# Performance work log

Hardware: AMD Instinct MI355X
Metric: run time of the kernel (lower is better)

Reference implementation:

```python
import jax, jax.numpy as jnp
import numpy as np

BITWIDTH = 8
SCALE = 2.0 ** (BITWIDTH - 1)  # bipolar SC quantization levels


def quantize(v):
    """SourceGen/BSGen over 2^bitwidth cycles converges to the bitwidth-quantized
    bipolar value in [-1, 1]; straight-through estimator keeps grads alive."""
    q = jnp.round(jnp.clip(v, -1.0, 1.0) * SCALE) / SCALE
    return v + jax.lax.stop_gradient(q - v)


def sc_clip(v):
    # non-scaled SC accumulation saturates the bipolar range [-1, 1]
    return jnp.clip(v, -1.0, 1.0)


def fsu_relu(v):
    # FSUReLU on bipolar streams: negative rates -> 0, stays in [0, 1]
    return jnp.clip(v, 0.0, 1.0)


def conv2d(x, w):
    # NCHW conv, padding=1, stride=1 (HUBConv2d / FSUConv2d rate-level math)
    return jax.lax.conv_general_dilated(
        x, w, window_strides=(1, 1), padding=[(1, 1), (1, 1)],
        dimension_numbers=("NCHW", "OIHW", "NCHW"))


def setup_inputs() -> dict:
    key = jax.random.key(0)
    ks = jax.random.split(key, 8)
    B, W, H, Wd = 2048, 10, 10, 11
    cnn_chn, fc_sz, hid, n_cls = 16, 256, 64, 7
    fc3_in = H * Wd * cnn_chn * 2  # 3520
    s = 0.1
    return {
        "x": jax.random.normal(ks[0], (B, W, H, Wd), jnp.float32) * 0.5,
        "conv1_w": jax.random.normal(ks[1], (cnn_chn, 1, 3, 3), jnp.float32) * s,
        "conv2_w": jax.random.normal(ks[2], (cnn_chn * 2, cnn_chn, 3, 3), jnp.float32) * s,
        "fc3_w": jax.random.normal(ks[3], (fc_sz, fc3_in), jnp.float32) * s,
        "w_ih": jax.random.normal(ks[4], (2 * hid, fc_sz), jnp.float32) * s,
        "w_hh": jax.random.normal(ks[5], (2 * hid, hid), jnp.float32) * s,
        "fc5_w": jax.random.normal(ks[6], (n_cls, hid), jnp.float32) * s,
    }


def _forward(x, conv1_w, conv2_w, fc3_w, w_ih, w_hh, fc5_w):
    B = x.shape[0]
    hid = w_hh.shape[1]

    def mgu_cell(x_t, hx):
        # FSUMGUCell, hard nonlinearities (rnn_hard=True)
        gi = x_t @ w_ih.T                         # [B, 2H]
        gh = hx @ w_hh.T                          # [B, 2H]
        gi_f, gi_n = jnp.split(gi, 2, axis=-1)
        gh_f, gh_n = jnp.split(gh, 2, axis=-1)
        forgetgate = jnp.clip(0.5 * (gi_f + gh_f) + 0.5, 0.0, 1.0)  # hard sigmoid
        newgate_prod = forgetgate * gh_n
        newgate = jnp.clip(gi_n + newgate_prod, -1.0, 1.0)          # hard tanh
        forgetgate_inv_prod = (1.0 - forgetgate) * newgate
        forgetgate_prod = forgetgate * hx
        return forgetgate_inv_prod + forgetgate_prod

    def step(hx, x_win):
        xi = quantize(x_win)[:, None, :, :]        # [B,1,10,11] bitstream rate
        a1 = fsu_relu(sc_clip(conv2d(xi, conv1_w)))
        a2 = fsu_relu(sc_clip(conv2d(a1, conv2_w)))
        f = a2.reshape(B, -1)                      # [B, 3520]
        a3 = fsu_relu(sc_clip(f @ fc3_w.T))        # [B, 256]
        hq = quantize(hx)
        hx_new = mgu_cell(a3, hq)
        return hx_new, None

    hx0 = jnp.zeros((B, hid), x.dtype)
    xs = jnp.transpose(x, (1, 0, 2, 3))            # [W, B, 10, 11]
    hx, _ = jax.lax.scan(step, hx0, xs)
    return hx @ fc5_w.T                            # [B, 7] fc5 logits


def reference(x, conv1_w, conv2_w, fc3_w, w_ih, w_hh, fc5_w):
    return _forward(x, conv1_w, conv2_w, fc3_w, w_ih, w_hh, fc5_w)
```

## Files before the change

kernel.cpp:

```cpp
#include <hip/hip_runtime.h>
#include <hip/hip_bf16.h>
#include <cstdint>
#include <cstddef>


typedef __bf16 bf16x8v __attribute__((ext_vector_type(8)));
typedef float  f32x4   __attribute__((ext_vector_type(4)));

#define WAVE_FENCE() asm volatile("s_waitcnt lgkmcnt(0)" ::: "memory")

#define A1_PS 24
#define A1_RS (13 * A1_PS)
#define A1_ZS (12 * A1_RS)
#define A1_BS 3776
#define XQ_BS 176

#define FC3_K 3584

__global__ __launch_bounds__(256) void cvt_w3p_k(
    const float* __restrict__ in, __hip_bfloat16* __restrict__ out)
{
    int idx = blockIdx.x * 256 + threadIdx.x;
    int n = idx / FC3_K, kp = idx % FC3_K;
    int mt = kp >> 9, r = kp & 511;
    int fq = r >> 7, col = (r >> 3) & 15, nt = (r >> 2) & 1, j = r & 3;
    int pixel = mt * 16 + fq * 4 + j, oc = nt * 16 + col;
    float v = (pixel < 110) ? in[n * 3520 + oc * 110 + pixel] : 0.f;
    out[idx] = __float2bfloat16(v);
}

__global__ __launch_bounds__(256) void cvt_w2p_k(
    const float* __restrict__ w2g, __hip_bfloat16* __restrict__ out)
{
    int idx = blockIdx.x * 256 + threadIdx.x;
    int oc = idx / 160, k = idx % 160;
    int koff = k >> 4, ic = k & 15;
    float v = (koff < 9) ? w2g[(oc * 16 + ic) * 9 + koff] : 0.f;
    out[idx] = __float2bfloat16(v);
}

__global__ __launch_bounds__(256) void cvt_wihfrag_k(
    const float* __restrict__ wih, __hip_bfloat16* __restrict__ out)
{
    int idx = blockIdx.x * 256 + threadIdx.x;
    int e = idx & 7, lane = (idx >> 3) & 63, hl = (idx >> 9) & 1;
    int kt = (idx >> 10) & 7, nt = (idx >> 13) & 7;
    int gate = nt * 16 + (lane & 15);
    int k = kt * 32 + (lane >> 4) * 8 + e;
    float v = wih[gate * 256 + k];
    __hip_bfloat16 hi = __float2bfloat16(v);
    out[idx] = hl ? __float2bfloat16(v - __bfloat162float(hi)) : hi;
}

__global__ __launch_bounds__(256) void cvt_whhfrag_k(
    const float* __restrict__ whh, __hip_bfloat16* __restrict__ out)
{
    int idx = blockIdx.x * 256 + threadIdx.x;
    int e = idx & 7, lane = (idx >> 3) & 63, hl = (idx >> 9) & 1;
    int kt = (idx >> 10) & 1, nt = (idx >> 11) & 7;
    int gate = nt * 16 + (lane & 15);
    int k = kt * 32 + (lane >> 4) * 8 + e;
    float v = whh[gate * 64 + k];
    __hip_bfloat16 hi = __float2bfloat16(v);
    out[idx] = hl ? __float2bfloat16(v - __bfloat162float(hi)) : hi;
}

__global__ __launch_bounds__(256) void conv_all_k(
    const float* __restrict__ x, const float* __restrict__ w1g,
    const __hip_bfloat16* __restrict__ w2p,
    __hip_bfloat16* __restrict__ a2p)
{
    __shared__ __hip_bfloat16 a1_s[4 * A1_BS];
    __shared__ float xq_s[4 * XQ_BS];

    const int tid  = threadIdx.x;
    const int wv   = tid >> 6, lane = tid & 63;
    const int t    = blockIdx.x >> 9;
    const int b    = (blockIdx.x & 511) * 4 + wv;
    const int ab   = wv * A1_BS;
    const int xb   = wv * XQ_BS;

    const int fr  = lane & 15, fq = lane >> 4;
    const int fqh = fq >> 1,  icb = (fq & 1) * 8;

    bf16x8v bfrag[5][2];
#pragma unroll
    for (int kt = 0; kt < 5; ++kt)
#pragma unroll
        for (int nt = 0; nt < 2; ++nt)
            bfrag[kt][nt] = *(const bf16x8v*)&w2p[(nt * 16 + fr) * 160 + kt * 32 + fq * 8];

    const int ocp = lane >> 3, pg = lane & 7;
    float w1a[9], w1b[9];
#pragma unroll
    for (int k = 0; k < 9; ++k) {
        w1a[k] = w1g[(2 * ocp) * 9 + k];
        w1b[k] = w1g[(2 * ocp + 1) * 9 + k];
    }

    {
        bf16x8v z = {};
#pragma unroll
        for (int i = 0; i < 8; ++i) {
            int c = lane + i * 64;
            if (c < A1_BS / 8) *(bf16x8v*)&a1_s[ab + c * 8] = z;
        }
        float4 zf = {0.f, 0.f, 0.f, 0.f};
        if (lane < XQ_BS / 4) *(float4*)&xq_s[xb + lane * 4] = zf;
    }
    WAVE_FENCE();

#pragma unroll
    for (int pass = 0; pass < 2; ++pass) {
        int p = pass * 64 + lane;
        if (p < 110) {
            float xv = x[(size_t)b * 1100 + t * 110 + p];
            xv = fminf(fmaxf(xv, -1.f), 1.f);
            xv = rintf(xv * 128.f) * 0.0078125f;
            int h = p / 11, w = p - h * 11;
            xq_s[xb + (h + 1) * 14 + (w + 1)] = xv;
        }
    }
    WAVE_FENCE();

#pragma unroll 2
    for (int i = 0; i < 14; ++i) {
        int p = pg * 14 + i;
        if (p < 110) {
            int h = p / 11, w = p - h * 11;
            const float* xw = &xq_s[xb + h * 14 + w];
            float a0 = 0.f, a1v = 0.f;
#pragma unroll
            for (int dr = 0; dr < 3; ++dr)
#pragma unroll
                for (int dc = 0; dc < 3; ++dc) {
                    float sv = xw[dr * 14 + dc];
                    a0  += w1a[dr * 3 + dc] * sv;
                    a1v += w1b[dr * 3 + dc] * sv;
                }
            a0  = fminf(fmaxf(a0, 0.f), 1.f);
            a1v = fminf(fmaxf(a1v, 0.f), 1.f);
            __hip_bfloat162 pr;
            pr.x = __float2bfloat16(a0);
            pr.y = __float2bfloat16(a1v);
            *(__hip_bfloat162*)&a1_s[ab + (h + 1) * A1_RS + (w + 1) * A1_PS + 2 * ocp] = pr;
        }
    }
    WAVE_FENCE();

    const int d0 = fqh * 24 + icb;
    const int d1 = (fqh ? 312 : 48) + icb;
    const int d2 = 336 + fqh * 24 + icb;
    const int d3 = 624 + fqh * 24 + icb;

#pragma unroll
    for (int m = 0; m < 7; ++m) {
        int p = m * 16 + fr; if (p > 109) p = 109;
        int h = p / 11, w = p - h * 11;
        const int bm = ab + h * A1_RS + w * A1_PS;
        f32x4 acc0 = {0.f, 0.f, 0.f, 0.f}, acc1 = {0.f, 0.f, 0.f, 0.f};
        bf16x8v a;
        a = *(const bf16x8v*)&a1_s[bm + d0];
        acc0 = __builtin_amdgcn_mfma_f32_16x16x32_bf16(a, bfrag[0][0], acc0, 0, 0, 0);
        acc1 = __builtin_amdgcn_mfma_f32_16x16x32_bf16(a, bfrag[0][1], acc1, 0, 0, 0);
        a = *(const bf16x8v*)&a1_s[bm + d1];
        acc0 = __builtin_amdgcn_mfma_f32_16x16x32_bf16(a, bfrag[1][0], acc0, 0, 0, 0);
        acc1 = __builtin_amdgcn_mfma_f32_16x16x32_bf16(a, bfrag[1][1], acc1, 0, 0, 0);
        a = *(const bf16x8v*)&a1_s[bm + d2];
        acc0 = __builtin_amdgcn_mfma_f32_16x16x32_bf16(a, bfrag[2][0], acc0, 0, 0, 0);
        acc1 = __builtin_amdgcn_mfma_f32_16x16x32_bf16(a, bfrag[2][1], acc1, 0, 0, 0);
        a = *(const bf16x8v*)&a1_s[bm + d3];
        acc0 = __builtin_amdgcn_mfma_f32_16x16x32_bf16(a, bfrag[3][0], acc0, 0, 0, 0);
        acc1 = __builtin_amdgcn_mfma_f32_16x16x32_bf16(a, bfrag[3][1], acc1, 0, 0, 0);
        a = *(const bf16x8v*)&a1_s[fqh ? (ab + A1_ZS) : (bm + 672 + icb)];
        acc0 = __builtin_amdgcn_mfma_f32_16x16x32_bf16(a, bfrag[4][0], acc0, 0, 0, 0);
        acc1 = __builtin_amdgcn_mfma_f32_16x16x32_bf16(a, bfrag[4][1], acc1, 0, 0, 0);

        bf16x8v ov;
#pragma unroll
        for (int j = 0; j < 4; ++j) {
            bool valid = (m * 16 + fq * 4 + j) < 110;
            float v0 = valid ? fminf(fmaxf(acc0[j], 0.f), 1.f) : 0.f;
            float v1 = valid ? fminf(fmaxf(acc1[j], 0.f), 1.f) : 0.f;
            ov[j]     = (__bf16)v0;
            ov[4 + j] = (__bf16)v1;
        }
        *(bf16x8v*)&a2p[(size_t)(t * 2048 + b) * FC3_K + m * 512 + lane * 8] = ov;
    }
}

__global__ __launch_bounds__(256) void fc3_all_k(
    const __hip_bfloat16* __restrict__ A,
    const __hip_bfloat16* __restrict__ W,
    __hip_bfloat16* __restrict__ a3)
{
    __shared__ __hip_bfloat16 As[128 * 64];
    __shared__ __hip_bfloat16 Bs[64 * 64];

    const int tid  = threadIdx.x;
    const int wv   = tid >> 6;
    const int lane = tid & 63;
    const int m0 = blockIdx.x * 128, n0 = blockIdx.y * 64;
    const int wr = wv >> 1, wc = wv & 1;

    const int srow   = lane >> 3;
    const int schunk = lane & 7;
    const int swzc   = schunk ^ srow;

    const int fr = lane & 15;
    const int fq = lane >> 4;

    f32x4 acc[4][2];
#pragma unroll
    for (int mi = 0; mi < 4; ++mi)
#pragma unroll
        for (int ni = 0; ni < 2; ++ni)
            acc[mi][ni] = (f32x4){0.f, 0.f, 0.f, 0.f};

    for (int kt = 0; kt < 56; ++kt) {
        const int kb = kt * 64;
#pragma unroll
        for (int i = 0; i < 4; ++i) {
            const int tr = wv * 32 + i * 8;
            const __hip_bfloat16* srcA =
                A + (size_t)(m0 + tr + srow) * FC3_K + kb + swzc * 8;
            __builtin_amdgcn_global_load_lds(
                (const __attribute__((address_space(1))) void*)srcA,
                (__attribute__((address_space(3))) void*)&As[tr * 64], 16, 0, 0);
        }
#pragma unroll
        for (int i = 0; i < 2; ++i) {
            const int tr = wv * 16 + i * 8;
            const __hip_bfloat16* srcB =
                W + (size_t)(n0 + tr + srow) * FC3_K + kb + swzc * 8;
            __builtin_amdgcn_global_load_lds(
                (const __attribute__((address_space(1))) void*)srcB,
                (__attribute__((address_space(3))) void*)&Bs[tr * 64], 16, 0, 0);
        }
        __syncthreads();

#pragma unroll
        for (int kk = 0; kk < 2; ++kk) {
            bf16x8v af[4], bfv[2];
#pragma unroll
            for (int mi = 0; mi < 4; ++mi) {
                const int rr = wr * 64 + mi * 16 + fr;
                const int cc = (kk * 4 + fq) ^ (rr & 7);
                af[mi] = *(const bf16x8v*)&As[rr * 64 + cc * 8];
            }
#pragma unroll
            for (int ni = 0; ni < 2; ++ni) {
                const int rr = wc * 32 + ni * 16 + fr;
                const int cc = (kk * 4 + fq) ^ (rr & 7);
                bfv[ni] = *(const bf16x8v*)&Bs[rr * 64 + cc * 8];
            }
#pragma unroll
            for (int mi = 0; mi < 4; ++mi)
#pragma unroll
                for (int ni = 0; ni < 2; ++ni)
                    acc[mi][ni] = __builtin_amdgcn_mfma_f32_16x16x32_bf16(
                        af[mi], bfv[ni], acc[mi][ni], 0, 0, 0);
        }
        __syncthreads();
    }

#pragma unroll
    for (int mi = 0; mi < 4; ++mi)
#pragma unroll
        for (int ni = 0; ni < 2; ++ni)
#pragma unroll
            for (int j = 0; j < 4; ++j) {
                int row = m0 + wr * 64 + mi * 16 + fq * 4 + j;
                int col = n0 + wc * 32 + ni * 16 + fr;
                float v = fminf(fmaxf(acc[mi][ni][j], 0.f), 1.f);
                a3[(size_t)row * 256 + col] = __float2bfloat16(v);
            }
}

__global__ __launch_bounds__(256, 1) void mgu_all_k(
    const __hip_bfloat16* __restrict__ a3,
    const __hip_bfloat16* __restrict__ wfi, const __hip_bfloat16* __restrict__ wfh,
    const float* __restrict__ w5, float* __restrict__ out)
{
    __shared__ __hip_bfloat16 a3_s[16 * 256];
    __shared__ __hip_bfloat16 hq_s[16 * 64];
    __shared__ float hx_s[16 * 64];
    __shared__ float w5_s[7 * 64];

    const int tid = threadIdx.x;
    const int wv  = tid >> 6, lane = tid & 63;
    const int fr  = lane & 15, fq = lane >> 4;
    const int b0  = blockIdx.x * 16;
    const int ntf = wv, ntn = wv + 4;

    bf16x8v wiF[8][2], wiN[8][2], whF[2][2], whN[2][2];
#pragma unroll
    for (int kt = 0; kt < 8; ++kt)
#pragma unroll
        for (int hl = 0; hl < 2; ++hl) {
            wiF[kt][hl] = *(const bf16x8v*)&wfi[(((ntf * 8 + kt) * 2 + hl) * 64 + lane) * 8];
            wiN[kt][hl] = *(const bf16x8v*)&wfi[(((ntn * 8 + kt) * 2 + hl) * 64 + lane) * 8];
        }
#pragma unroll
    for (int kt = 0; kt < 2; ++kt)
#pragma unroll
        for (int hl = 0; hl < 2; ++hl) {
            whF[kt][hl] = *(const bf16x8v*)&wfh[(((ntf * 2 + kt) * 2 + hl) * 64 + lane) * 8];
            whN[kt][hl] = *(const bf16x8v*)&wfh[(((ntn * 2 + kt) * 2 + hl) * 64 + lane) * 8];
        }

    for (int i = tid; i < 16 * 64; i += 256) hx_s[i] = 0.f;
    for (int i = tid; i < 7 * 64; i += 256) w5_s[i] = w5[i];
    __syncthreads();

    for (int t = 0; t < 10; ++t) {
#pragma unroll
        for (int pass = 0; pass < 2; ++pass) {
            int i = pass * 256 + tid;
            int r = i >> 5, cq = i & 31;
            bf16x8v v = *(const bf16x8v*)&a3[((size_t)(t * 2048 + b0 + r)) * 256 + cq * 8];
            *(bf16x8v*)&a3_s[r * 256 + ((cq ^ (r & 7)) * 8)] = v;
        }
#pragma unroll
        for (int pass = 0; pass < 4; ++pass) {
            int i = pass * 256 + tid;
            int r = i >> 6, c = i & 63;
            float v = hx_s[r * 64 + c];
            v = fminf(fmaxf(v, -1.f), 1.f);
            v = rintf(v * 128.f) * 0.0078125f;
            hq_s[r * 64 + (((c >> 3) ^ (r & 7)) << 3) + (c & 7)] = __float2bfloat16(v);
        }
        __syncthreads();

        f32x4 accF  = {0.f, 0.f, 0.f, 0.f};
        f32x4 accNi = {0.f, 0.f, 0.f, 0.f};
        f32x4 accNh = {0.f, 0.f, 0.f, 0.f};
#pragma unroll
        for (int kt = 0; kt < 8; ++kt) {
            bf16x8v a = *(const bf16x8v*)&a3_s[fr * 256 + (((kt * 4 + fq) ^ (fr & 7)) * 8)];
            accF  = __builtin_amdgcn_mfma_f32_16x16x32_bf16(a, wiF[kt][0], accF, 0, 0, 0);
            accF  = __builtin_amdgcn_mfma_f32_16x16x32_bf16(a, wiF[kt][1], accF, 0, 0, 0);
            accNi = __builtin_amdgcn_mfma_f32_16x16x32_bf16(a, wiN[kt][0], accNi, 0, 0, 0);
            accNi = __builtin_amdgcn_mfma_f32_16x16x32_bf16(a, wiN[kt][1], accNi, 0, 0, 0);
        }
#pragma unroll
        for (int kt = 0; kt < 2; ++kt) {
            bf16x8v a = *(const bf16x8v*)&hq_s[fr * 64 + (((kt * 4 + fq) ^ (fr & 7)) * 8)];
            accF  = __builtin_amdgcn_mfma_f32_16x16x32_bf16(a, whF[kt][0], accF, 0, 0, 0);
            accF  = __builtin_amdgcn_mfma_f32_16x16x32_bf16(a, whF[kt][1], accF, 0, 0, 0);
            accNh = __builtin_amdgcn_mfma_f32_16x16x32_bf16(a, whN[kt][0], accNh, 0, 0, 0);
            accNh = __builtin_amdgcn_mfma_f32_16x16x32_bf16(a, whN[kt][1], accNh, 0, 0, 0);
        }

        const int j5 = wv * 16 + fr;
#pragma unroll
        for (int j = 0; j < 4; ++j) {
            int b = fq * 4 + j;
            float f = fminf(fmaxf(0.5f * accF[j] + 0.5f, 0.f), 1.f);
            float n = fminf(fmaxf(accNi[j] + f * accNh[j], -1.f), 1.f);
            float hq = __bfloat162float(
                hq_s[b * 64 + ((((j5) >> 3) ^ (b & 7)) << 3) + (j5 & 7)]);
            hx_s[b * 64 + j5] = (1.f - f) * n + f * hq;
        }
        __syncthreads();
    }

    if (tid < 112) {
        int b = tid / 7, c = tid % 7;
        float acc = 0.f;
#pragma unroll
        for (int k = 0; k < 64; ++k) acc += hx_s[b * 64 + k] * w5_s[c * 64 + k];
        out[(size_t)(b0 + b) * 7 + c] = acc;
    }
}

extern "C" void kernel_launch(void* const* d_in, const int* in_sizes, int n_in,
                              void* d_out, int out_size, void* d_ws, size_t ws_size,
                              hipStream_t stream)
{
    const float* x    = (const float*)d_in[0];
    const float* w1   = (const float*)d_in[1];
    const float* w2   = (const float*)d_in[2];
    const float* fc3w = (const float*)d_in[3];
    const float* wih  = (const float*)d_in[4];
    const float* whh  = (const float*)d_in[5];
    const float* fc5w = (const float*)d_in[6];
    float* out = (float*)d_out;

    char* ws = (char*)d_ws;
    __hip_bfloat16* a2p = (__hip_bfloat16*)ws;
    __hip_bfloat16* a3  = (__hip_bfloat16*)(ws + 146800640);
    __hip_bfloat16* w3p = (__hip_bfloat16*)(ws + 157286400);
    __hip_bfloat16* w2p = (__hip_bfloat16*)(ws + 159121408);
    __hip_bfloat16* wfi = (__hip_bfloat16*)(ws + 159131648);
    __hip_bfloat16* wfh = (__hip_bfloat16*)(ws + 159262720);

    cvt_w3p_k<<<3584, 256, 0, stream>>>(fc3w, w3p);
    cvt_w2p_k<<<20, 256, 0, stream>>>(w2, w2p);
    cvt_wihfrag_k<<<256, 256, 0, stream>>>(wih, wfi);
    cvt_whhfrag_k<<<64, 256, 0, stream>>>(whh, wfh);

    conv_all_k<<<5120, 256, 0, stream>>>(x, w1, w2p, a2p);
    fc3_all_k<<<dim3(160, 4), 256, 0, stream>>>(a2p, w3p, a3);
    mgu_all_k<<<128, 256, 0, stream>>>(a3, wfi, wfh, fc5w, out);
}
```

Baseline: 120.8 us.

## Double-buffer fc3 GEMM loads, fuse weight conversions, row-tile conv1, swap grid order

The fc3 GEMM now double-buffers its LDS tiles, issuing the next k-tile's direct-to-LDS loads before computing the current one and waiting with vmcnt. This overlaps global memory latency with MFMA work. The four weight-conversion kernels are merged into one launch to cut launch overhead. conv1 now computes whole output rows per lane from vectorised float4 row loads instead of scattered per-pixel reads. The fc3 grid is transposed so the four N-blocks sharing an A tile run adjacently, improving L2 reuse; LDS use doubles.

```diff
diff --git a/kernel.cpp b/kernel.cpp
--- a/kernel.cpp
+++ b/kernel.cpp
@@ -13,56 +13,53 @@
 #define A1_RS (13 * A1_PS)
 #define A1_ZS (12 * A1_RS)
 #define A1_BS 3776
-#define XQ_BS 176
+#define XQ_RS 20
+#define XQ_BS 256
 
 #define FC3_K 3584
 
-__global__ __launch_bounds__(256) void cvt_w3p_k(
-    const float* __restrict__ in, __hip_bfloat16* __restrict__ out)
+__global__ __launch_bounds__(256) void cvt_all_k(
+    const float* __restrict__ fc3w, const float* __restrict__ w2g,
+    const float* __restrict__ wih,  const float* __restrict__ whh,
+    __hip_bfloat16* __restrict__ w3p, __hip_bfloat16* __restrict__ w2p,
+    __hip_bfloat16* __restrict__ wfi, __hip_bfloat16* __restrict__ wfh)
 {
-    int idx = blockIdx.x * 256 + threadIdx.x;
-    int n = idx / FC3_K, kp = idx % FC3_K;
-    int mt = kp >> 9, r = kp & 511;
-    int fq = r >> 7, col = (r >> 3) & 15, nt = (r >> 2) & 1, j = r & 3;
-    int pixel = mt * 16 + fq * 4 + j, oc = nt * 16 + col;
-    float v = (pixel < 110) ? in[n * 3520 + oc * 110 + pixel] : 0.f;
-    out[idx] = __float2bfloat16(v);
-}
-
-__global__ __launch_bounds__(256) void cvt_w2p_k(
-    const float* __restrict__ w2g, __hip_bfloat16* __restrict__ out)
-{
-    int idx = blockIdx.x * 256 + threadIdx.x;
-    int oc = idx / 160, k = idx % 160;
-    int koff = k >> 4, ic = k & 15;
-    float v = (koff < 9) ? w2g[(oc * 16 + ic) * 9 + koff] : 0.f;
-    out[idx] = __float2bfloat16(v);
-}
-
-__global__ __launch_bounds__(256) void cvt_wihfrag_k(
-    const float* __restrict__ wih, __hip_bfloat16* __restrict__ out)
-{
-    int idx = blockIdx.x * 256 + threadIdx.x;
-    int e = idx & 7, lane = (idx >> 3) & 63, hl = (idx >> 9) & 1;
-    int kt = (idx >> 10) & 7, nt = (idx >> 13) & 7;
-    int gate = nt * 16 + (lane & 15);
-    int k = kt * 32 + (lane >> 4) * 8 + e;
-    float v = wih[gate * 256 + k];
-    __hip_bfloat16 hi = __float2bfloat16(v);
-    out[idx] = hl ? __float2bfloat16(v - __bfloat162float(hi)) : hi;
-}
-
-__global__ __launch_bounds__(256) void cvt_whhfrag_k(
-    const float* __restrict__ whh, __hip_bfloat16* __restrict__ out)
-{
-    int idx = blockIdx.x * 256 + threadIdx.x;
-    int e = idx & 7, lane = (idx >> 3) & 63, hl = (idx >> 9) & 1;
-    int kt = (idx >> 10) & 1, nt = (idx >> 11) & 7;
-    int gate = nt * 16 + (lane & 15);
-    int k = kt * 32 + (lane >> 4) * 8 + e;
-    float v = whh[gate * 64 + k];
-    __hip_bfloat16 hi = __float2bfloat16(v);
-    out[idx] = hl ? __float2bfloat16(v - __bfloat162float(hi)) : hi;
+    int bid = blockIdx.x;
+    if (bid < 3584) {
+        int idx = bid * 256 + threadIdx.x;
+        int n = idx / FC3_K, kp = idx % FC3_K;
+        int mt = kp >> 9, r = kp & 511;
+        int fq = r >> 7, col = (r >> 3) & 15, nt = (r >> 2) & 1, j = r & 3;
+        int pixel = mt * 16 + fq * 4 + j, oc = nt * 16 + col;
+        float v = (pixel < 110) ? fc3w[n * 3520 + oc * 110 + pixel] : 0.f;
+        w3p[idx] = __float2bfloat16(v);
+    } else if (bid < 3604) {
+        int idx = (bid - 3584) * 256 + threadIdx.x;
+        if (idx < 5120) {
+            int oc = idx / 160, k = idx % 160;
+            int koff = k >> 4, ic = k & 15;
+            float v = (koff < 9) ? w2g[(oc * 16 + ic) * 9 + koff] : 0.f;
+            w2p[idx] = __float2bfloat16(v);
+        }
+    } else if (bid < 3860) {
+        int idx = (bid - 3604) * 256 + threadIdx.x;
+        int e = idx & 7, lane = (idx >> 3) & 63, hl = (idx >> 9) & 1;
+        int kt = (idx >> 10) & 7, nt = (idx >> 13) & 7;
+        int gate = nt * 16 + (lane & 15);
+        int k = kt * 32 + (lane >> 4) * 8 + e;
+        float v = wih[gate * 256 + k];
+        __hip_bfloat16 hi = __float2bfloat16(v);
+        wfi[idx] = hl ? __float2bfloat16(v - __bfloat162float(hi)) : hi;
+    } else {
+        int idx = (bid - 3860) * 256 + threadIdx.x;
+        int e = idx & 7, lane = (idx >> 3) & 63, hl = (idx >> 9) & 1;
+        int kt = (idx >> 10) & 1, nt = (idx >> 11) & 7;
+        int gate = nt * 16 + (lane & 15);
+        int k = kt * 32 + (lane >> 4) * 8 + e;
+        float v = whh[gate * 64 + k];
+        __hip_bfloat16 hi = __float2bfloat16(v);
+        wfh[idx] = hl ? __float2bfloat16(v - __bfloat162float(hi)) : hi;
+    }
 }
 
 __global__ __launch_bounds__(256) void conv_all_k(
@@ -90,7 +87,7 @@
         for (int nt = 0; nt < 2; ++nt)
             bfrag[kt][nt] = *(const bf16x8v*)&w2p[(nt * 16 + fr) * 160 + kt * 32 + fq * 8];
 
-    const int ocp = lane >> 3, pg = lane & 7;
+    const int ocp = lane & 7, rs = lane >> 3;
     float w1a[9], w1b[9];
 #pragma unroll
     for (int k = 0; k < 9; ++k) {
@@ -106,7 +103,7 @@
             if (c < A1_BS / 8) *(bf16x8v*)&a1_s[ab + c * 8] = z;
         }
         float4 zf = {0.f, 0.f, 0.f, 0.f};
-        if (lane < XQ_BS / 4) *(float4*)&xq_s[xb + lane * 4] = zf;
+        *(float4*)&xq_s[xb + lane * 4] = zf;
     }
     WAVE_FENCE();
 
@@ -118,32 +115,42 @@
             xv = fminf(fmaxf(xv, -1.f), 1.f);
             xv = rintf(xv * 128.f) * 0.0078125f;
             int h = p / 11, w = p - h * 11;
-            xq_s[xb + (h + 1) * 14 + (w + 1)] = xv;
+            xq_s[xb + (h + 1) * XQ_RS + (w + 1)] = xv;
         }
     }
     WAVE_FENCE();
 
-#pragma unroll 2
-    for (int i = 0; i < 14; ++i) {
-        int p = pg * 14 + i;
-        if (p < 110) {
-            int h = p / 11, w = p - h * 11;
-            const float* xw = &xq_s[xb + h * 14 + w];
-            float a0 = 0.f, a1v = 0.f;
-#pragma unroll
-            for (int dr = 0; dr < 3; ++dr)
+#pragma unroll
+    for (int pass = 0; pass < 2; ++pass) {
+        const int hr = pass == 0 ? rs : rs + 8;
+        if (hr < 10) {
+            float acc0[11], acc1[11];
+#pragma unroll
+            for (int w = 0; w < 11; ++w) { acc0[w] = 0.f; acc1[w] = 0.f; }
+#pragma unroll
+            for (int dr = 0; dr < 3; ++dr) {
+                float xr[16];
+                const float* row = &xq_s[xb + (hr + dr) * XQ_RS];
+#pragma unroll
+                for (int j = 0; j < 4; ++j)
+                    *(float4*)&xr[j * 4] = *(const float4*)&row[j * 4];
 #pragma unroll
                 for (int dc = 0; dc < 3; ++dc) {
-                    float sv = xw[dr * 14 + dc];
-                    a0  += w1a[dr * 3 + dc] * sv;
-                    a1v += w1b[dr * 3 + dc] * sv;
+                    float wa = w1a[dr * 3 + dc], wb = w1b[dr * 3 + dc];
+#pragma unroll
+                    for (int w = 0; w < 11; ++w) {
+                        acc0[w] += xr[w + dc] * wa;
+                        acc1[w] += xr[w + dc] * wb;
+                    }
                 }
-            a0  = fminf(fmaxf(a0, 0.f), 1.f);
-            a1v = fminf(fmaxf(a1v, 0.f), 1.f);
-            __hip_bfloat162 pr;
-            pr.x = __float2bfloat16(a0);
-            pr.y = __float2bfloat16(a1v);
-            *(__hip_bfloat162*)&a1_s[ab + (h + 1) * A1_RS + (w + 1) * A1_PS + 2 * ocp] = pr;
+            }
+#pragma unroll
+            for (int w = 0; w < 11; ++w) {
+                __hip_bfloat162 pr;
+                pr.x = __float2bfloat16(fminf(fmaxf(acc0[w], 0.f), 1.f));
+                pr.y = __float2bfloat16(fminf(fmaxf(acc1[w], 0.f), 1.f));
+                *(__hip_bfloat162*)&a1_s[ab + (hr + 1) * A1_RS + (w + 1) * A1_PS + 2 * ocp] = pr;
+            }
         }
     }
     WAVE_FENCE();
@@ -194,13 +201,13 @@
     const __hip_bfloat16* __restrict__ W,
     __hip_bfloat16* __restrict__ a3)
 {
-    __shared__ __hip_bfloat16 As[128 * 64];
-    __shared__ __hip_bfloat16 Bs[64 * 64];
+    __shared__ __hip_bfloat16 As[2 * 128 * 64];
+    __shared__ __hip_bfloat16 Bs[2 * 64 * 64];
 
     const int tid  = threadIdx.x;
     const int wv   = tid >> 6;
     const int lane = tid & 63;
-    const int m0 = blockIdx.x * 128, n0 = blockIdx.y * 64;
+    const int m0 = blockIdx.y * 128, n0 = blockIdx.x * 64;
     const int wr = wv >> 1, wc = wv & 1;
 
     const int srow   = lane >> 3;
@@ -217,7 +224,7 @@
         for (int ni = 0; ni < 2; ++ni)
             acc[mi][ni] = (f32x4){0.f, 0.f, 0.f, 0.f};
 
-    for (int kt = 0; kt < 56; ++kt) {
+    auto STAGE = [&](int kt, int pb) {
         const int kb = kt * 64;
 #pragma unroll
         for (int i = 0; i < 4; ++i) {
@@ -226,7 +233,7 @@
                 A + (size_t)(m0 + tr + srow) * FC3_K + kb + swzc * 8;
             __builtin_amdgcn_global_load_lds(
                 (const __attribute__((address_space(1))) void*)srcA,
-                (__attribute__((address_space(3))) void*)&As[tr * 64], 16, 0, 0);
+                (__attribute__((address_space(3))) void*)&As[pb * 8192 + tr * 64], 16, 0, 0);
         }
 #pragma unroll
         for (int i = 0; i < 2; ++i) {
@@ -235,10 +242,23 @@
                 W + (size_t)(n0 + tr + srow) * FC3_K + kb + swzc * 8;
             __builtin_amdgcn_global_load_lds(
                 (const __attribute__((address_space(1))) void*)srcB,
-                (__attribute__((address_space(3))) void*)&Bs[tr * 64], 16, 0, 0);
-        }
-        __syncthreads();
-
+                (__attribute__((address_space(3))) void*)&Bs[pb * 4096 + tr * 64], 16, 0, 0);
+        }
+    };
+
+    STAGE(0, 0);
+    int cur = 0;
+    for (int kt = 0; kt < 56; ++kt) {
+        if (kt + 1 < 56) {
+            STAGE(kt + 1, cur ^ 1);
+            asm volatile("s_waitcnt vmcnt(6)" ::: "memory");
+        } else {
+            asm volatile("s_waitcnt vmcnt(0)" ::: "memory");
+        }
+        __builtin_amdgcn_s_barrier();
+
+        const __hip_bfloat16* Ab = &As[cur * 8192];
+        const __hip_bfloat16* Bb = &Bs[cur * 4096];
 #pragma unroll
         for (int kk = 0; kk < 2; ++kk) {
             bf16x8v af[4], bfv[2];
@@ -246,13 +266,13 @@
             for (int mi = 0; mi < 4; ++mi) {
                 const int rr = wr * 64 + mi * 16 + fr;
                 const int cc = (kk * 4 + fq) ^ (rr & 7);
-                af[mi] = *(const bf16x8v*)&As[rr * 64 + cc * 8];
+                af[mi] = *(const bf16x8v*)&Ab[rr * 64 + cc * 8];
             }
 #pragma unroll
             for (int ni = 0; ni < 2; ++ni) {
                 const int rr = wc * 32 + ni * 16 + fr;
                 const int cc = (kk * 4 + fq) ^ (rr & 7);
-                bfv[ni] = *(const bf16x8v*)&Bs[rr * 64 + cc * 8];
+                bfv[ni] = *(const bf16x8v*)&Bb[rr * 64 + cc * 8];
             }
 #pragma unroll
             for (int mi = 0; mi < 4; ++mi)
@@ -261,7 +281,8 @@
                     acc[mi][ni] = __builtin_amdgcn_mfma_f32_16x16x32_bf16(
                         af[mi], bfv[ni], acc[mi][ni], 0, 0, 0);
         }
-        __syncthreads();
+        __builtin_amdgcn_s_barrier();
+        cur ^= 1;
     }
 
 #pragma unroll
@@ -395,12 +416,8 @@
     __hip_bfloat16* wfi = (__hip_bfloat16*)(ws + 159131648);
     __hip_bfloat16* wfh = (__hip_bfloat16*)(ws + 159262720);
 
-    cvt_w3p_k<<<3584, 256, 0, stream>>>(fc3w, w3p);
-    cvt_w2p_k<<<20, 256, 0, stream>>>(w2, w2p);
-    cvt_wihfrag_k<<<256, 256, 0, stream>>>(wih, wfi);
-    cvt_whhfrag_k<<<64, 256, 0, stream>>>(whh, wfh);
-
+    cvt_all_k<<<3924, 256, 0, stream>>>(fc3w, w2, wih, whh, w3p, w2p, wfi, wfh);
     conv_all_k<<<5120, 256, 0, stream>>>(x, w1, w2p, a2p);
-    fc3_all_k<<<dim3(160, 4), 256, 0, stream>>>(a2p, w3p, a3);
+    fc3_all_k<<<dim3(4, 160), 256, 0, stream>>>(a2p, w3p, a3);
     mgu_all_k<<<128, 256, 0, stream>>>(a3, wfi, wfh, fc5w, out);
 }
```

Result: slower. 146.8 us (+21.5%).
